# Kernel optimization log

Measured on AMD Instinct MI355X. Metric: run time of the kernel, lower is better.

The kernel has to match this reference:

```python
import jax, jax.numpy as jnp
import numpy as np

N = 50000
E = 640000
DIM_NODE = 128
DIM_HIDDEN = 128
DIM_FFN = 512
NUM_CLASSES = 10
NUM_GRAPHS = 128
NEG_SLOPE = 0.2


def setup_inputs() -> dict:
    key = jax.random.key(0)
    ks = jax.random.split(key, 24)
    g = lambda k, shape: jax.random.normal(k, shape, dtype=jnp.float32) * 0.05
    inp = {
        "x": jax.random.normal(ks[0], (N, DIM_NODE), dtype=jnp.float32),
        "edge_index": jax.random.randint(ks[1], (2, E), 0, N, dtype=jnp.int64),
        "batch": jnp.sort(jax.random.randint(ks[2], (N,), 0, NUM_GRAPHS, dtype=jnp.int64)),
        # GATConv 1: dim_node -> dim_hidden (heads=1)
        "W1": g(ks[3], (DIM_NODE, DIM_HIDDEN)),
        "as1": g(ks[4], (DIM_HIDDEN,)), "ad1": g(ks[5], (DIM_HIDDEN,)),
        "b1": g(ks[6], (DIM_HIDDEN,)),
        # GATConv 2
        "W2": g(ks[7], (DIM_HIDDEN, DIM_HIDDEN)),
        "as2": g(ks[8], (DIM_HIDDEN,)), "ad2": g(ks[9], (DIM_HIDDEN,)),
        "b2": g(ks[10], (DIM_HIDDEN,)),
        # GATConv 3
        "W3": g(ks[11], (DIM_HIDDEN, DIM_HIDDEN)),
        "as3": g(ks[12], (DIM_HIDDEN,)), "ad3": g(ks[13], (DIM_HIDDEN,)),
        "b3": g(ks[14], (DIM_HIDDEN,)),
        # FFN head
        "Wf1": g(ks[15], (DIM_HIDDEN, DIM_FFN)), "bf1": g(ks[16], (DIM_FFN,)),
        "Wf2": g(ks[17], (DIM_FFN, DIM_FFN)), "bf2": g(ks[18], (DIM_FFN,)),
        "Wf3": g(ks[19], (DIM_FFN, NUM_CLASSES)), "bf3": g(ks[20], (NUM_CLASSES,)),
    }
    return inp


def _gat_conv(x, src, dst, W, a_src, a_dst, bias):
    # x: [N, Fin]; src/dst: [E'] (self-loops included)
    h = x @ W                                  # [N, H]
    alpha_src = h @ a_src                      # [N]
    alpha_dst = h @ a_dst                      # [N]
    logits = jax.nn.leaky_relu(alpha_src[src] + alpha_dst[dst], NEG_SLOPE)  # [E']
    # segment softmax over incoming edges of each dst node
    m = jax.ops.segment_max(logits, dst, num_segments=N)
    ex = jnp.exp(logits - m[dst])
    denom = jax.ops.segment_sum(ex, dst, num_segments=N)
    alpha = ex / (denom[dst] + 1e-16)          # [E']
    out = jax.ops.segment_sum(alpha[:, None] * h[src], dst, num_segments=N)
    return out + bias


def reference(x, edge_index, batch, W1, as1, ad1, b1, W2, as2, ad2, b2,
              W3, as3, ad3, b3, Wf1, bf1, Wf2, bf2, Wf3, bf3):
    # PyG GATConv adds self-loops by default
    loops = jnp.arange(N, dtype=edge_index.dtype)
    src = jnp.concatenate([edge_index[0], loops])
    dst = jnp.concatenate([edge_index[1], loops])

    h = jax.nn.relu(_gat_conv(x, src, dst, W1, as1, ad1, b1))
    h = jax.nn.relu(_gat_conv(h, src, dst, W2, as2, ad2, b2))
    h = jax.nn.relu(_gat_conv(h, src, dst, W3, as3, ad3, b3))

    # global mean pool per graph
    sums = jax.ops.segment_sum(h, batch, num_segments=NUM_GRAPHS)
    cnts = jax.ops.segment_sum(jnp.ones((N,), h.dtype), batch, num_segments=NUM_GRAPHS)
    pooled = sums / jnp.maximum(cnts, 1.0)[:, None]   # [G, H]

    # FFN head (dropout is identity in eval)
    z = jax.nn.relu(pooled @ Wf1 + bf1)
    z = jax.nn.relu(z @ Wf2 + bf2)
    return z @ Wf3 + bf3                               # [G, num_classes]
```

## Files before the change

### kernel.cpp

```cpp
#include <hip/hip_runtime.h>

#define N_NODES 50000
#define N_EDGES 640000
#define TOT_E (N_EDGES + N_NODES)
#define NB 196
#define BCAP 4608
#define EPW 4096
#define NG 128
#define NCLS 10
#define NEG 0.2f
#define PCHUNK 50

typedef unsigned int u32;
typedef unsigned short u16;
typedef __attribute__((ext_vector_type(8))) short s16x8;
typedef __attribute__((ext_vector_type(4))) float f32x4;

__device__ inline u32 bf16rne(float f) {
  u32 u = __float_as_uint(f);
  return (u + 0x7FFFu + ((u >> 16) & 1u)) >> 16;
}
__device__ inline float bf2f(u16 v) { return __uint_as_float((u32)v << 16); }

__global__ __launch_bounds__(256) void prep_kernel(int* __restrict__ bcur,
                                                   float* __restrict__ psum,
                                                   float* __restrict__ pcnt,
                                                   const float* __restrict__ W0,
                                                   const float* __restrict__ W1,
                                                   const float* __restrict__ W2,
                                                   u16* __restrict__ Wt,
                                                   const float* __restrict__ Wf3,
                                                   float* __restrict__ Wf3t) {
  int i = blockIdx.x * 256 + threadIdx.x;
  if (i < NB) bcur[i] = 0;
  if (i < NG * 128) psum[i] = 0.f;
  if (i < NG) pcnt[i] = 0.f;
  if (i < 3 * 128 * 128) {
    int l = i >> 14, c = (i >> 7) & 127, k = i & 127;
    const float* W = (l == 0) ? W0 : ((l == 1) ? W1 : W2);
    Wt[i] = (u16)bf16rne(W[k * 128 + c]);
  } else if (i < 3 * 128 * 128 + NCLS * 512) {
    int j = i - 3 * 128 * 128;
    int c = j >> 9, k = j & 511;
    Wf3t[j] = Wf3[k * NCLS + c];
  }
}

__global__ __launch_bounds__(256) void scatter_kernel(const int* __restrict__ ei,
                                                      int* __restrict__ bcur,
                                                      u32* __restrict__ ebuf) {
  __shared__ int hist[NB], basee[NB], lcur[NB];
  int t = threadIdx.x;
  for (int b = t; b < NB; b += 256) hist[b] = 0;
  __syncthreads();
  int e0 = blockIdx.x * EPW;
  int e1 = min(TOT_E, e0 + EPW);
  for (int e = e0 + t; e < e1; e += 256) {
    int d = (e < N_EDGES) ? ei[N_EDGES + e] : (e - N_EDGES);
    atomicAdd(&hist[d >> 8], 1);
  }
  __syncthreads();
  for (int b = t; b < NB; b += 256) {
    int c = hist[b];
    basee[b] = (c > 0) ? atomicAdd(&bcur[b], c) : 0;
    lcur[b] = 0;
  }
  __syncthreads();
  for (int e = e0 + t; e < e1; e += 256) {
    int d, s;
    if (e < N_EDGES) { d = ei[N_EDGES + e]; s = ei[e]; }
    else { d = e - N_EDGES; s = d; }
    int b = d >> 8;
    int r = basee[b] + atomicAdd(&lcur[b], 1);
    if (r < BCAP) ebuf[(size_t)b * BCAP + r] = ((u32)d << 16) | (u32)s;
  }
}

__global__ __launch_bounds__(256) void degfill_kernel(const int* __restrict__ bcur,
                                                      const u32* __restrict__ ebuf,
                                                      u32* __restrict__ rldeg,
                                                      u16* __restrict__ col) {
  __shared__ int cnt[256], s[256], cur[256];
  int b = blockIdx.x, t = threadIdx.x;
  cnt[t] = 0; __syncthreads();
  int n = min(bcur[b], BCAP);
  const u32* eb = ebuf + (size_t)b * BCAP;
  for (int i = t; i < n; i += 256) atomicAdd(&cnt[(eb[i] >> 16) & 255], 1);
  __syncthreads();
  int v = cnt[t];
  s[t] = v; __syncthreads();
  for (int off = 1; off < 256; off <<= 1) {
    int tmp = (t >= off) ? s[t - off] : 0;
    __syncthreads();
    s[t] += tmp;
    __syncthreads();
  }
  int rl = s[t] - v;
  int node = (b << 8) + t;
  if (node < N_NODES) rldeg[node] = ((u32)rl << 16) | (u32)v;
  cur[t] = rl;
  __syncthreads();
  u16* cb = col + (size_t)b * BCAP;
  for (int i = t; i < n; i += 256) {
    u32 p = eb[i];
    int pos = atomicAdd(&cur[(p >> 16) & 255], 1);
    cb[pos] = (u16)(p & 0xFFFFu);
  }
}

template <bool CVT>
__global__ __launch_bounds__(64) void gemm_mfma(const void* __restrict__ Xin,
                                                const u16* __restrict__ Wt,
                                                const float* __restrict__ avs,
                                                const float* __restrict__ avd,
                                                u16* __restrict__ Hb,
                                                float* __restrict__ as_out,
                                                float* __restrict__ ad_out) {
  __shared__ u16 st[16 * 128];
  int lane = threadIdx.x;
  int m0 = blockIdx.x * 16;
  int ar = lane & 15, kg = lane >> 4;
  f32x4 acc[8];
#pragma unroll
  for (int n = 0; n < 8; n++) acc[n] = (f32x4){0.f, 0.f, 0.f, 0.f};
#pragma unroll
  for (int ks = 0; ks < 4; ks++) {
    s16x8 a;
    if (CVT) {
      const float* xr = (const float*)Xin + (size_t)(m0 + ar) * 128 + ks * 32 + kg * 8;
      float4 f0 = *(const float4*)xr;
      float4 f1 = *(const float4*)(xr + 4);
      a[0] = (short)bf16rne(f0.x); a[1] = (short)bf16rne(f0.y);
      a[2] = (short)bf16rne(f0.z); a[3] = (short)bf16rne(f0.w);
      a[4] = (short)bf16rne(f1.x); a[5] = (short)bf16rne(f1.y);
      a[6] = (short)bf16rne(f1.z); a[7] = (short)bf16rne(f1.w);
    } else {
      a = *(const s16x8*)((const u16*)Xin + (size_t)(m0 + ar) * 128 + ks * 32 + kg * 8);
    }
#pragma unroll
    for (int n = 0; n < 8; n++) {
      s16x8 b = *(const s16x8*)(Wt + (size_t)(n * 16 + ar) * 128 + ks * 32 + kg * 8);
      acc[n] = __builtin_amdgcn_mfma_f32_16x16x32_bf16(a, b, acc[n], 0, 0, 0);
    }
  }
  float avsv[8], advv[8];
#pragma unroll
  for (int n = 0; n < 8; n++) { avsv[n] = avs[n * 16 + ar]; advv[n] = avd[n * 16 + ar]; }
#pragma unroll
  for (int reg = 0; reg < 4; reg++) {
    float ps = 0.f, pd = 0.f;
#pragma unroll
    for (int n = 0; n < 8; n++) {
      ps = fmaf(acc[n][reg], avsv[n], ps);
      pd = fmaf(acc[n][reg], advv[n], pd);
    }
#pragma unroll
    for (int off = 1; off < 16; off <<= 1) {
      ps += __shfl_xor(ps, off, 64);
      pd += __shfl_xor(pd, off, 64);
    }
    if (ar == 0) {
      int row = m0 + kg * 4 + reg;
      as_out[row] = ps; ad_out[row] = pd;
    }
  }
#pragma unroll
  for (int n = 0; n < 8; n++)
#pragma unroll
    for (int reg = 0; reg < 4; reg++)
      st[(kg * 4 + reg) * 128 + n * 16 + ar] = (u16)bf16rne(acc[n][reg]);
  __syncthreads();
#pragma unroll
  for (int i = 0; i < 4; i++) {
    int u4 = i * 64 + lane;
    int r = u4 >> 4;
    int c8 = (u4 & 15) * 8;
    *(uint4*)(Hb + (size_t)(m0 + r) * 128 + c8) = *(const uint4*)&st[r * 128 + c8];
  }
}

__global__ __launch_bounds__(256) void agg_kernel(
    const u16* __restrict__ Hb, const float* __restrict__ asv,
    const float* __restrict__ adv, const u32* __restrict__ rldeg,
    const u16* __restrict__ col, const float* __restrict__ bias,
    u16* __restrict__ Ob) {
  int gid = blockIdx.x * blockDim.x + threadIdx.x;
  int node = gid >> 6;
  if (node >= N_NODES) return;
  int lane = threadIdx.x & 63;
  int q = lane >> 4;
  int li = lane & 15;
  u32 rd = rldeg[node];
  int r0 = (node >> 8) * BCAP + (int)(rd >> 16);
  int r1 = r0 + (int)(rd & 0xFFFFu);
  float ad = adv[node];
  float acc[8];
#pragma unroll
  for (int k = 0; k < 8; k++) acc[k] = 0.f;
  float den = 0.f;

  for (int base = r0; base < r1; base += 64) {
    int cnt = min(64, r1 - base);
    int s_l = 0; float ex_l = 0.f;
    if (lane < cnt) {
      s_l = (int)col[base + lane];
      float tt = asv[s_l] + ad;
      tt = (tt > 0.f) ? tt : NEG * tt;
      ex_l = __expf(tt);
    }
    float d = ex_l;
#pragma unroll
    for (int off = 32; off; off >>= 1) d += __shfl_xor(d, off, 64);
    den += d;

    int j = 0;
    for (; j + 8 <= cnt; j += 8) {
      int i0 = j + q, i1 = j + 4 + q;
      int s0 = __shfl(s_l, i0, 64); float e0 = __shfl(ex_l, i0, 64);
      int s1 = __shfl(s_l, i1, 64); float e1 = __shfl(ex_l, i1, 64);
      uint4 h0 = *(const uint4*)(Hb + (size_t)s0 * 128 + li * 8);
      uint4 h1 = *(const uint4*)(Hb + (size_t)s1 * 128 + li * 8);
      u32 w0[4] = {h0.x, h0.y, h0.z, h0.w};
      u32 w1[4] = {h1.x, h1.y, h1.z, h1.w};
#pragma unroll
      for (int k = 0; k < 4; k++) {
        acc[2 * k]     = fmaf(e0, __uint_as_float(w0[k] << 16), acc[2 * k]);
        acc[2 * k + 1] = fmaf(e0, __uint_as_float(w0[k] & 0xFFFF0000u), acc[2 * k + 1]);
      }
#pragma unroll
      for (int k = 0; k < 4; k++) {
        acc[2 * k]     = fmaf(e1, __uint_as_float(w1[k] << 16), acc[2 * k]);
        acc[2 * k + 1] = fmaf(e1, __uint_as_float(w1[k] & 0xFFFF0000u), acc[2 * k + 1]);
      }
    }
    for (; j < cnt; j += 4) {
      int i0 = j + q;
      int s0 = __shfl(s_l, i0, 64); float e0 = __shfl(ex_l, i0, 64);
      if (i0 < cnt) {
        uint4 h0 = *(const uint4*)(Hb + (size_t)s0 * 128 + li * 8);
        u32 w0[4] = {h0.x, h0.y, h0.z, h0.w};
#pragma unroll
        for (int k = 0; k < 4; k++) {
          acc[2 * k]     = fmaf(e0, __uint_as_float(w0[k] << 16), acc[2 * k]);
          acc[2 * k + 1] = fmaf(e0, __uint_as_float(w0[k] & 0xFFFF0000u), acc[2 * k + 1]);
        }
      }
    }
  }
#pragma unroll
  for (int k = 0; k < 8; k++) {
    acc[k] += __shfl_xor(acc[k], 16, 64);
    acc[k] += __shfl_xor(acc[k], 32, 64);
  }

  if (q == 0) {
    float inv = 1.f / (den + 1e-16f);
    float4 b0 = *(const float4*)(bias + li * 8);
    float4 b1 = *(const float4*)(bias + li * 8 + 4);
    float o[8];
    o[0] = fmaxf(fmaf(acc[0], inv, b0.x), 0.f);
    o[1] = fmaxf(fmaf(acc[1], inv, b0.y), 0.f);
    o[2] = fmaxf(fmaf(acc[2], inv, b0.z), 0.f);
    o[3] = fmaxf(fmaf(acc[3], inv, b0.w), 0.f);
    o[4] = fmaxf(fmaf(acc[4], inv, b1.x), 0.f);
    o[5] = fmaxf(fmaf(acc[5], inv, b1.y), 0.f);
    o[6] = fmaxf(fmaf(acc[6], inv, b1.z), 0.f);
    o[7] = fmaxf(fmaf(acc[7], inv, b1.w), 0.f);
    uint4 pb;
    pb.x = bf16rne(o[0]) | (bf16rne(o[1]) << 16);
    pb.y = bf16rne(o[2]) | (bf16rne(o[3]) << 16);
    pb.z = bf16rne(o[4]) | (bf16rne(o[5]) << 16);
    pb.w = bf16rne(o[6]) | (bf16rne(o[7]) << 16);
    *(uint4*)(Ob + (size_t)node * 128 + li * 8) = pb;
  }
}

__global__ void pool_kernel(const u16* __restrict__ Hb, const int* __restrict__ batch,
                            float* __restrict__ psum, float* __restrict__ pcnt) {
  int t = threadIdx.x;
  int start = blockIdx.x * PCHUNK;
  int end = min(N_NODES, start + PCHUNK);
  if (start >= end) return;
  int cur = batch[start];
  float acc = 0.f; int cnt = 0;
  for (int i = start; i < end; ++i) {
    int g = batch[i];
    if (g != cur) {
      atomicAdd(&psum[cur * 128 + t], acc);
      if (t == 0) atomicAdd(&pcnt[cur], (float)cnt);
      acc = 0.f; cnt = 0; cur = g;
    }
    acc += bf2f(Hb[(size_t)i * 128 + t]);
    cnt++;
  }
  atomicAdd(&psum[cur * 128 + t], acc);
  if (t == 0) atomicAdd(&pcnt[cur], (float)cnt);
}

__global__ __launch_bounds__(128) void ffn1_kernel(const float* __restrict__ psum,
                                                   const float* __restrict__ pcnt,
                                                   const float* __restrict__ Wf1,
                                                   const float* __restrict__ bf1,
                                                   float* __restrict__ z1) {
  __shared__ float prow[128];
  int b = blockIdx.x;
  int g = b >> 2, ch = b & 3;
  int t = threadIdx.x;
  prow[t] = psum[g * 128 + t] / fmaxf(pcnt[g], 1.f);
  __syncthreads();
  int c = ch * 128 + t;
  float a = bf1[c];
#pragma unroll 8
  for (int k = 0; k < 128; ++k) a = fmaf(prow[k], Wf1[k * 512 + c], a);
  z1[g * 512 + c] = fmaxf(a, 0.f);
}

__global__ __launch_bounds__(256) void ffn2_kernel(const float* __restrict__ z1,
                                                   const float* __restrict__ Wf2,
                                                   const float* __restrict__ bf2,
                                                   float* __restrict__ z2) {
  __shared__ float z1s[512];
  __shared__ float part[256];
  int b = blockIdx.x;
  int g = b >> 3, ch = b & 7;
  int t = threadIdx.x;
  z1s[t] = z1[g * 512 + t];
  z1s[t + 256] = z1[g * 512 + t + 256];
  __syncthreads();
  int c = ch * 64 + (t & 63);
  int kq = t >> 6;
  float a = 0.f;
#pragma unroll 8
  for (int kk = 0; kk < 128; ++kk) {
    int k = kq * 128 + kk;
    a = fmaf(z1s[k], Wf2[k * 512 + c], a);
  }
  part[t] = a;
  __syncthreads();
  if (kq == 0) {
    float s = part[t] + part[t + 64] + part[t + 128] + part[t + 192] + bf2[c];
    z2[g * 512 + c] = fmaxf(s, 0.f);
  }
}

__global__ __launch_bounds__(256) void ffn3_kernel(const float* __restrict__ z2,
                                                   const float* __restrict__ Wf3t,
                                                   const float* __restrict__ bf3,
                                                   float* __restrict__ out) {
  int wid = blockIdx.x * 4 + (threadIdx.x >> 6);
  int lane = threadIdx.x & 63;
  int g = wid / NCLS, c = wid - g * NCLS;
  float a = 0.f;
#pragma unroll
  for (int j = 0; j < 8; ++j) {
    int k = j * 64 + lane;
    a = fmaf(z2[g * 512 + k], Wf3t[c * 512 + k], a);
  }
#pragma unroll
  for (int off = 32; off; off >>= 1) a += __shfl_xor(a, off, 64);
  if (lane == 0) out[g * NCLS + c] = a + bf3[c];
}

extern "C" void kernel_launch(void* const* d_in, const int* in_sizes, int n_in,
                              void* d_out, int out_size, void* d_ws, size_t ws_size,
                              hipStream_t stream) {
  const float* x   = (const float*)d_in[0];
  const int*   ei  = (const int*)d_in[1];
  const int*   bat = (const int*)d_in[2];
  const float* W[3]  = {(const float*)d_in[3], (const float*)d_in[7],  (const float*)d_in[11]};
  const float* As[3] = {(const float*)d_in[4], (const float*)d_in[8],  (const float*)d_in[12]};
  const float* Ad[3] = {(const float*)d_in[5], (const float*)d_in[9],  (const float*)d_in[13]};
  const float* B[3]  = {(const float*)d_in[6], (const float*)d_in[10], (const float*)d_in[14]};
  const float* Wf1 = (const float*)d_in[15]; const float* bf1 = (const float*)d_in[16];
  const float* Wf2 = (const float*)d_in[17]; const float* bf2 = (const float*)d_in[18];
  const float* Wf3 = (const float*)d_in[19]; const float* bf3 = (const float*)d_in[20];
  float* out = (float*)d_out;

  size_t off = 0;
  auto carve = [&](size_t bytes) {
    void* p = (char*)d_ws + off;
    off += (bytes + 255) & ~(size_t)255;
    return p;
  };
  u16*   Ab0    = (u16*)carve((size_t)N_NODES * 128 * 2);
  u16*   Ab1    = (u16*)carve((size_t)N_NODES * 128 * 2);
  u16*   Hb     = (u16*)carve((size_t)N_NODES * 128 * 2);
  u16*   Wt     = (u16*)carve((size_t)3 * 128 * 128 * 2);
  float* as_    = (float*)carve((size_t)N_NODES * 4);
  float* ad_    = (float*)carve((size_t)N_NODES * 4);
  u32*   rldeg  = (u32*)carve((size_t)N_NODES * 4);
  u16*   col    = (u16*)carve((size_t)NB * BCAP * 2);
  u32*   ebuf   = (u32*)carve((size_t)NB * BCAP * 4);
  int*   bcur   = (int*)carve(NB * 4);
  float* psum   = (float*)carve(NG * 128 * 4);
  float* pcnt   = (float*)carve(NG * 4);
  float* z1     = (float*)carve(NG * 512 * 4);
  float* z2     = (float*)carve(NG * 512 * 4);
  float* Wf3t   = (float*)carve((size_t)NCLS * 512 * 4);

  prep_kernel<<<256, 256, 0, stream>>>(bcur, psum, pcnt, W[0], W[1], W[2], Wt, Wf3, Wf3t);

  int sgrid = (TOT_E + EPW - 1) / EPW;
  scatter_kernel<<<sgrid, 256, 0, stream>>>(ei, bcur, ebuf);
  degfill_kernel<<<NB, 256, 0, stream>>>(bcur, ebuf, rldeg, col);

  int node_waves_grid = (N_NODES * 64 + 255) / 256;
  gemm_mfma<true><<<3125, 64, 0, stream>>>(x, Wt, As[0], Ad[0], Hb, as_, ad_);
  agg_kernel<<<node_waves_grid, 256, 0, stream>>>(Hb, as_, ad_, rldeg, col, B[0], Ab0);
  gemm_mfma<false><<<3125, 64, 0, stream>>>(Ab0, Wt + 16384, As[1], Ad[1], Hb, as_, ad_);
  agg_kernel<<<node_waves_grid, 256, 0, stream>>>(Hb, as_, ad_, rldeg, col, B[1], Ab1);
  gemm_mfma<false><<<3125, 64, 0, stream>>>(Ab1, Wt + 32768, As[2], Ad[2], Hb, as_, ad_);
  agg_kernel<<<node_waves_grid, 256, 0, stream>>>(Hb, as_, ad_, rldeg, col, B[2], Ab0);

  pool_kernel<<<(N_NODES + PCHUNK - 1) / PCHUNK, 128, 0, stream>>>(Ab0, bat, psum, pcnt);
  ffn1_kernel<<<NG * 4, 128, 0, stream>>>(psum, pcnt, Wf1, bf1, z1);
  ffn2_kernel<<<NG * 8, 256, 0, stream>>>(z1, Wf2, bf2, z2);
  ffn3_kernel<<<320, 256, 0, stream>>>(z2, Wf3t, bf3, out);
}
```

Measured before the change: 228.1 us.

## Store transformed features as FP8 and fuse mean-pool into final aggregation

The GEMM now writes the projected node features as FP8 instead of bf16, which halves the bytes the aggregation kernel gathers per edge. The aggregation unpacks them with the hardware fp8-to-f32 conversion. The separate pool kernel is removed: the last aggregation atomically adds each node's output straight into the per-graph sums. Graph counts are now found by binary search over the sorted batch array inside ffn1. FP8 storage loses precision compared with bf16, and per-node float atomics on 128 graph rows may contend.

After: 560.3 us. 2.46x slower.

```diff
diff --git a/kernel.cpp b/kernel.cpp
--- a/kernel.cpp
+++ b/kernel.cpp
@@ -9,22 +9,36 @@
 #define NG 128
 #define NCLS 10
 #define NEG 0.2f
-#define PCHUNK 50
 
 typedef unsigned int u32;
 typedef unsigned short u16;
+typedef unsigned char u8;
 typedef __attribute__((ext_vector_type(8))) short s16x8;
 typedef __attribute__((ext_vector_type(4))) float f32x4;
+typedef __attribute__((ext_vector_type(2))) float f32x2;
 
 __device__ inline u32 bf16rne(float f) {
   u32 u = __float_as_uint(f);
   return (u + 0x7FFFu + ((u >> 16) & 1u)) >> 16;
 }
-__device__ inline float bf2f(u16 v) { return __uint_as_float((u32)v << 16); }
+
+__device__ inline void acc_fp8x8(float e, uint2 h, float* acc) {
+  f32x2 p0 = __builtin_amdgcn_cvt_pk_f32_fp8((int)h.x, false);
+  f32x2 p1 = __builtin_amdgcn_cvt_pk_f32_fp8((int)h.x, true);
+  f32x2 p2 = __builtin_amdgcn_cvt_pk_f32_fp8((int)h.y, false);
+  f32x2 p3 = __builtin_amdgcn_cvt_pk_f32_fp8((int)h.y, true);
+  acc[0] = fmaf(e, p0[0], acc[0]);
+  acc[1] = fmaf(e, p0[1], acc[1]);
+  acc[2] = fmaf(e, p1[0], acc[2]);
+  acc[3] = fmaf(e, p1[1], acc[3]);
+  acc[4] = fmaf(e, p2[0], acc[4]);
+  acc[5] = fmaf(e, p2[1], acc[5]);
+  acc[6] = fmaf(e, p3[0], acc[6]);
+  acc[7] = fmaf(e, p3[1], acc[7]);
+}
 
 __global__ __launch_bounds__(256) void prep_kernel(int* __restrict__ bcur,
                                                    float* __restrict__ psum,
-                                                   float* __restrict__ pcnt,
                                                    const float* __restrict__ W0,
                                                    const float* __restrict__ W1,
                                                    const float* __restrict__ W2,
@@ -34,7 +48,6 @@
   int i = blockIdx.x * 256 + threadIdx.x;
   if (i < NB) bcur[i] = 0;
   if (i < NG * 128) psum[i] = 0.f;
-  if (i < NG) pcnt[i] = 0.f;
   if (i < 3 * 128 * 128) {
     int l = i >> 14, c = (i >> 7) & 127, k = i & 127;
     const float* W = (l == 0) ? W0 : ((l == 1) ? W1 : W2);
@@ -113,10 +126,10 @@
                                                 const u16* __restrict__ Wt,
                                                 const float* __restrict__ avs,
                                                 const float* __restrict__ avd,
-                                                u16* __restrict__ Hb,
+                                                u8* __restrict__ Hf8,
                                                 float* __restrict__ as_out,
                                                 float* __restrict__ ad_out) {
-  __shared__ u16 st[16 * 128];
+  __shared__ __align__(16) u8 st8[16 * 128];
   int lane = threadIdx.x;
   int m0 = blockIdx.x * 16;
   int ar = lane & 15, kg = lane >> 4;
@@ -167,23 +180,26 @@
 #pragma unroll
   for (int n = 0; n < 8; n++)
 #pragma unroll
-    for (int reg = 0; reg < 4; reg++)
-      st[(kg * 4 + reg) * 128 + n * 16 + ar] = (u16)bf16rne(acc[n][reg]);
-  __syncthreads();
-#pragma unroll
-  for (int i = 0; i < 4; i++) {
-    int u4 = i * 64 + lane;
-    int r = u4 >> 4;
-    int c8 = (u4 & 15) * 8;
-    *(uint4*)(Hb + (size_t)(m0 + r) * 128 + c8) = *(const uint4*)&st[r * 128 + c8];
+    for (int reg = 0; reg < 4; reg++) {
+      float v = acc[n][reg];
+      u32 p = (u32)__builtin_amdgcn_cvt_pk_fp8_f32(v, v, 0, false);
+      st8[(kg * 4 + reg) * 128 + n * 16 + ar] = (u8)(p & 0xFFu);
+    }
+  __syncthreads();
+#pragma unroll
+  for (int i = 0; i < 2; i++) {
+    int idx = i * 64 + lane;
+    int r = idx >> 3;
+    int c16 = (idx & 7) * 16;
+    *(uint4*)(Hf8 + (size_t)(m0 + r) * 128 + c16) = *(const uint4*)&st8[r * 128 + c16];
   }
 }
 
 __global__ __launch_bounds__(256) void agg_kernel(
-    const u16* __restrict__ Hb, const float* __restrict__ asv,
+    const u8* __restrict__ Hf8, const float* __restrict__ asv,
     const float* __restrict__ adv, const u32* __restrict__ rldeg,
     const u16* __restrict__ col, const float* __restrict__ bias,
-    u16* __restrict__ Ob) {
+    u16* __restrict__ Ob, float* __restrict__ psum, const int* __restrict__ batch) {
   int gid = blockIdx.x * blockDim.x + threadIdx.x;
   int node = gid >> 6;
   if (node >= N_NODES) return;
@@ -218,32 +234,17 @@
       int i0 = j + q, i1 = j + 4 + q;
       int s0 = __shfl(s_l, i0, 64); float e0 = __shfl(ex_l, i0, 64);
       int s1 = __shfl(s_l, i1, 64); float e1 = __shfl(ex_l, i1, 64);
-      uint4 h0 = *(const uint4*)(Hb + (size_t)s0 * 128 + li * 8);
-      uint4 h1 = *(const uint4*)(Hb + (size_t)s1 * 128 + li * 8);
-      u32 w0[4] = {h0.x, h0.y, h0.z, h0.w};
-      u32 w1[4] = {h1.x, h1.y, h1.z, h1.w};
-#pragma unroll
-      for (int k = 0; k < 4; k++) {
-        acc[2 * k]     = fmaf(e0, __uint_as_float(w0[k] << 16), acc[2 * k]);
-        acc[2 * k + 1] = fmaf(e0, __uint_as_float(w0[k] & 0xFFFF0000u), acc[2 * k + 1]);
-      }
-#pragma unroll
-      for (int k = 0; k < 4; k++) {
-        acc[2 * k]     = fmaf(e1, __uint_as_float(w1[k] << 16), acc[2 * k]);
-        acc[2 * k + 1] = fmaf(e1, __uint_as_float(w1[k] & 0xFFFF0000u), acc[2 * k + 1]);
-      }
+      uint2 h0 = *(const uint2*)(Hf8 + (size_t)s0 * 128 + li * 8);
+      uint2 h1 = *(const uint2*)(Hf8 + (size_t)s1 * 128 + li * 8);
+      acc_fp8x8(e0, h0, acc);
+      acc_fp8x8(e1, h1, acc);
     }
     for (; j < cnt; j += 4) {
       int i0 = j + q;
       int s0 = __shfl(s_l, i0, 64); float e0 = __shfl(ex_l, i0, 64);
       if (i0 < cnt) {
-        uint4 h0 = *(const uint4*)(Hb + (size_t)s0 * 128 + li * 8);
-        u32 w0[4] = {h0.x, h0.y, h0.z, h0.w};
-#pragma unroll
-        for (int k = 0; k < 4; k++) {
-          acc[2 * k]     = fmaf(e0, __uint_as_float(w0[k] << 16), acc[2 * k]);
-          acc[2 * k + 1] = fmaf(e0, __uint_as_float(w0[k] & 0xFFFF0000u), acc[2 * k + 1]);
-        }
+        uint2 h0 = *(const uint2*)(Hf8 + (size_t)s0 * 128 + li * 8);
+        acc_fp8x8(e0, h0, acc);
       }
     }
   }
@@ -266,39 +267,30 @@
     o[5] = fmaxf(fmaf(acc[5], inv, b1.y), 0.f);
     o[6] = fmaxf(fmaf(acc[6], inv, b1.z), 0.f);
     o[7] = fmaxf(fmaf(acc[7], inv, b1.w), 0.f);
-    uint4 pb;
-    pb.x = bf16rne(o[0]) | (bf16rne(o[1]) << 16);
-    pb.y = bf16rne(o[2]) | (bf16rne(o[3]) << 16);
-    pb.z = bf16rne(o[4]) | (bf16rne(o[5]) << 16);
-    pb.w = bf16rne(o[6]) | (bf16rne(o[7]) << 16);
-    *(uint4*)(Ob + (size_t)node * 128 + li * 8) = pb;
-  }
-}
-
-__global__ void pool_kernel(const u16* __restrict__ Hb, const int* __restrict__ batch,
-                            float* __restrict__ psum, float* __restrict__ pcnt) {
-  int t = threadIdx.x;
-  int start = blockIdx.x * PCHUNK;
-  int end = min(N_NODES, start + PCHUNK);
-  if (start >= end) return;
-  int cur = batch[start];
-  float acc = 0.f; int cnt = 0;
-  for (int i = start; i < end; ++i) {
-    int g = batch[i];
-    if (g != cur) {
-      atomicAdd(&psum[cur * 128 + t], acc);
-      if (t == 0) atomicAdd(&pcnt[cur], (float)cnt);
-      acc = 0.f; cnt = 0; cur = g;
-    }
-    acc += bf2f(Hb[(size_t)i * 128 + t]);
-    cnt++;
-  }
-  atomicAdd(&psum[cur * 128 + t], acc);
-  if (t == 0) atomicAdd(&pcnt[cur], (float)cnt);
+    if (psum) {
+      int g = batch[node];
+      float* p = psum + (size_t)g * 128 + li * 8;
+#pragma unroll
+      for (int k = 0; k < 8; k++) atomicAdd(p + k, o[k]);
+    } else {
+      uint4 pb;
+      pb.x = bf16rne(o[0]) | (bf16rne(o[1]) << 16);
+      pb.y = bf16rne(o[2]) | (bf16rne(o[3]) << 16);
+      pb.z = bf16rne(o[4]) | (bf16rne(o[5]) << 16);
+      pb.w = bf16rne(o[6]) | (bf16rne(o[7]) << 16);
+      *(uint4*)(Ob + (size_t)node * 128 + li * 8) = pb;
+    }
+  }
+}
+
+__device__ inline int lbound(const int* b, int n, int v) {
+  int lo = 0, hi = n;
+  while (lo < hi) { int m = (lo + hi) >> 1; if (b[m] < v) lo = m + 1; else hi = m; }
+  return lo;
 }
 
 __global__ __launch_bounds__(128) void ffn1_kernel(const float* __restrict__ psum,
-                                                   const float* __restrict__ pcnt,
+                                                   const int* __restrict__ batch,
                                                    const float* __restrict__ Wf1,
                                                    const float* __restrict__ bf1,
                                                    float* __restrict__ z1) {
@@ -306,7 +298,9 @@
   int b = blockIdx.x;
   int g = b >> 2, ch = b & 3;
   int t = threadIdx.x;
-  prow[t] = psum[g * 128 + t] / fmaxf(pcnt[g], 1.f);
+  int lo = lbound(batch, N_NODES, g), hi = lbound(batch, N_NODES, g + 1);
+  float cnt = fmaxf((float)(hi - lo), 1.f);
+  prow[t] = psum[g * 128 + t] / cnt;
   __syncthreads();
   int c = ch * 128 + t;
   float a = bf1[c];
@@ -384,7 +378,7 @@
   };
   u16*   Ab0    = (u16*)carve((size_t)N_NODES * 128 * 2);
   u16*   Ab1    = (u16*)carve((size_t)N_NODES * 128 * 2);
-  u16*   Hb     = (u16*)carve((size_t)N_NODES * 128 * 2);
+  u8*    Hf8    = (u8*)carve((size_t)N_NODES * 128);
   u16*   Wt     = (u16*)carve((size_t)3 * 128 * 128 * 2);
   float* as_    = (float*)carve((size_t)N_NODES * 4);
   float* ad_    = (float*)carve((size_t)N_NODES * 4);
@@ -393,27 +387,28 @@
   u32*   ebuf   = (u32*)carve((size_t)NB * BCAP * 4);
   int*   bcur   = (int*)carve(NB * 4);
   float* psum   = (float*)carve(NG * 128 * 4);
-  float* pcnt   = (float*)carve(NG * 4);
   float* z1     = (float*)carve(NG * 512 * 4);
   float* z2     = (float*)carve(NG * 512 * 4);
   float* Wf3t   = (float*)carve((size_t)NCLS * 512 * 4);
 
-  prep_kernel<<<256, 256, 0, stream>>>(bcur, psum, pcnt, W[0], W[1], W[2], Wt, Wf3, Wf3t);
+  prep_kernel<<<256, 256, 0, stream>>>(bcur, psum, W[0], W[1], W[2], Wt, Wf3, Wf3t);
 
   int sgrid = (TOT_E + EPW - 1) / EPW;
   scatter_kernel<<<sgrid, 256, 0, stream>>>(ei, bcur, ebuf);
   degfill_kernel<<<NB, 256, 0, stream>>>(bcur, ebuf, rldeg, col);
 
   int node_waves_grid = (N_NODES * 64 + 255) / 256;
-  gemm_mfma<true><<<3125, 64, 0, stream>>>(x, Wt, As[0], Ad[0], Hb, as_, ad_);
-  agg_kernel<<<node_waves_grid, 256, 0, stream>>>(Hb, as_, ad_, rldeg, col, B[0], Ab0);
-  gemm_mfma<false><<<3125, 64, 0, stream>>>(Ab0, Wt + 16384, As[1], Ad[1], Hb, as_, ad_);
-  agg_kernel<<<node_waves_grid, 256, 0, stream>>>(Hb, as_, ad_, rldeg, col, B[1], Ab1);
-  gemm_mfma<false><<<3125, 64, 0, stream>>>(Ab1, Wt + 32768, As[2], Ad[2], Hb, as_, ad_);
-  agg_kernel<<<node_waves_grid, 256, 0, stream>>>(Hb, as_, ad_, rldeg, col, B[2], Ab0);
-
-  pool_kernel<<<(N_NODES + PCHUNK - 1) / PCHUNK, 128, 0, stream>>>(Ab0, bat, psum, pcnt);
-  ffn1_kernel<<<NG * 4, 128, 0, stream>>>(psum, pcnt, Wf1, bf1, z1);
+  gemm_mfma<true><<<3125, 64, 0, stream>>>(x, Wt, As[0], Ad[0], Hf8, as_, ad_);
+  agg_kernel<<<node_waves_grid, 256, 0, stream>>>(Hf8, as_, ad_, rldeg, col, B[0],
+                                                  Ab0, nullptr, nullptr);
+  gemm_mfma<false><<<3125, 64, 0, stream>>>(Ab0, Wt + 16384, As[1], Ad[1], Hf8, as_, ad_);
+  agg_kernel<<<node_waves_grid, 256, 0, stream>>>(Hf8, as_, ad_, rldeg, col, B[1],
+                                                  Ab1, nullptr, nullptr);
+  gemm_mfma<false><<<3125, 64, 0, stream>>>(Ab1, Wt + 32768, As[2], Ad[2], Hf8, as_, ad_);
+  agg_kernel<<<node_waves_grid, 256, 0, stream>>>(Hf8, as_, ad_, rldeg, col, B[2],
+                                                  nullptr, psum, bat);
+
+  ffn1_kernel<<<NG * 4, 128, 0, stream>>>(psum, bat, Wf1, bf1, z1);
   ffn2_kernel<<<NG * 8, 256, 0, stream>>>(z1, Wf2, bf2, z2);
   ffn3_kernel<<<320, 256, 0, stream>>>(z2, Wf3t, bf3, out);
 }
```
